# Performance work log

Measured on AMD Instinct MI355X. Metric: run time of the kernel, lower is better.

The kernel has to match this reference:

```python
import jax, jax.numpy as jnp
import numpy as np

NH, NKV, HD = 32, 8, 64  # num heads, num kv heads, head_dim


def apply_rope(x, fc):
    # x: [B,S,H,D], fc: [S, D//2, 2]
    b, s, h, d = x.shape
    xr = x.reshape(b, s, h, d // 2, 2)
    fc = fc.reshape(1, s, 1, d // 2, 2)
    out = jnp.stack([
        xr[..., 0] * fc[..., 0] - xr[..., 1] * fc[..., 1],
        xr[..., 1] * fc[..., 0] + xr[..., 0] * fc[..., 1],
    ], axis=-1)
    return out.reshape(b, s, h, d)


def setup_inputs() -> dict:
    key = jax.random.key(0)
    k0, k1, k2 = jax.random.split(key, 3)
    B, S, H = 1, 2048, 2048
    x = jax.random.normal(k0, (B, S, H), jnp.float32)
    # rotary cos/sin table: [S, HD//2, 2]
    pos = jnp.arange(S, dtype=jnp.float32)
    inv_freq = 1.0 / (10000.0 ** (jnp.arange(0, HD, 2, dtype=jnp.float32) / HD))
    ang = pos[:, None] * inv_freq[None, :]
    freqs_cis = jnp.stack([jnp.cos(ang), jnp.sin(ang)], axis=-1)
    # causal bool mask [1,1,S,S]
    mask = jnp.tril(jnp.ones((S, S), dtype=bool))[None, None]
    scale = H ** -0.5
    Wqkv = jax.random.normal(k1, ((NH + 2 * NKV) * HD, H), jnp.float32) * scale
    Wo = jax.random.normal(k2, (H, H), jnp.float32) * scale
    return {"x": x, "freqs_cis": freqs_cis, "mask": mask, "Wqkv": Wqkv, "Wo": Wo}


def reference(x, freqs_cis, mask, Wqkv, Wo):
    B, S, H = x.shape
    g = NH // NKV  # GQA group size
    qkv = x @ Wqkv.T  # [B,S,(NH+2*NKV)*HD]
    q, k, v = jnp.split(qkv, [NH * HD, NH * HD + NKV * HD], axis=-1)
    q = q.reshape(B, S, NH, HD)
    k = k.reshape(B, S, NKV, HD)
    v = v.reshape(B, S, NKV, HD)
    q = apply_rope(q, freqs_cis)
    k = apply_rope(k, freqs_cis)
    # group query heads by shared kv head instead of repeat_interleave on K/V
    q = q.reshape(B, S, NKV, g, HD)
    scores = jnp.einsum('bskgd,btkd->bkgst', q, k) * (HD ** -0.5)
    scores = jnp.where(mask.reshape(1, 1, 1, S, S), scores, -jnp.inf)
    p = jax.nn.softmax(scores, axis=-1)
    y = jnp.einsum('bkgst,btkd->bskgd', p, v).reshape(B, S, H)
    return y @ Wo.T
```

## Files before the change

### kernel.cpp

```cpp
#include <hip/hip_runtime.h>
#include <stdint.h>

typedef unsigned short ushort_t;
typedef __attribute__((ext_vector_type(8))) short s8v;
typedef __attribute__((ext_vector_type(4))) float f4v;

#define NH 32
#define NKV 8
#define HD 64
#define S_LEN 2048
#define HID 2048
#define DQKV 3072

#define QSCALE 0.18033688011112042f

__device__ __forceinline__ ushort_t f2b(float f) {
  union { float f; unsigned u; } v; v.f = f;
  unsigned r = v.u + 0x7FFFu + ((v.u >> 16) & 1u);
  return (ushort_t)(r >> 16);
}
__device__ __forceinline__ float b2f(ushort_t h) {
  union { unsigned u; float f; } v; v.u = ((unsigned)h) << 16;
  return v.f;
}
__device__ __forceinline__ unsigned cvtpk(float lo, float hi) {
  unsigned r;
  asm("v_cvt_pk_bf16_f32 %0, %1, %2" : "=v"(r) : "v"(lo), "v"(hi));
  return r;
}

__global__ void cvt3(const float* __restrict__ a, const float* __restrict__ b,
                     const float* __restrict__ c, ushort_t* __restrict__ oa,
                     ushort_t* __restrict__ ob, ushort_t* __restrict__ oc) {
  const int n1 = 1048576, n2 = 1572864;
  int i = blockIdx.x * blockDim.x + threadIdx.x;
  const float* in; ushort_t* out; int j;
  if (i < n1) { in = a; out = oa; j = i; }
  else if (i < n1 + n2) { in = b; out = ob; j = i - n1; }
  else { in = c; out = oc; j = i - n1 - n2; }
  float4 v = ((const float4*)in)[j];
  uint2 p;
  p.x = cvtpk(v.x, v.y);
  p.y = cvtpk(v.z, v.w);
  ((uint2*)out)[j] = p;
}

__global__ __launch_bounds__(256) void gemm_bt_sk(
    const ushort_t* __restrict__ A, const ushort_t* __restrict__ B,
    ushort_t* __restrict__ C0, ushort_t* __restrict__ C1, int M, int N, int K) {
  __shared__ ushort_t sA[128 * 32];
  __shared__ ushort_t sB[128 * 32];
  const int tid = threadIdx.x;
  const int wave = tid >> 6, lane = tid & 63;
  const int bm = blockIdx.y * 128, bn = blockIdx.x * 128;
  const int wm = (wave >> 1) * 64, wn = (wave & 1) * 64;
  const int srow = wave * 16 + (lane >> 2);
  const int scol = (lane & 3) * 8;
  const int fr = lane & 15, fg = lane >> 4;
  const int khalf = K >> 1;
  const int kbeg = blockIdx.z * khalf;
  ushort_t* C = blockIdx.z ? C1 : C0;

  f4v acc[4][4];
#pragma unroll
  for (int m = 0; m < 4; ++m)
#pragma unroll
    for (int n = 0; n < 4; ++n) acc[m][n] = (f4v){0.f, 0.f, 0.f, 0.f};

  for (int k0 = kbeg; k0 < kbeg + khalf; k0 += 32) {
    __syncthreads();
#pragma unroll
    for (int it = 0; it < 2; ++it) {
      int r = it * 64 + srow;
      __builtin_amdgcn_global_load_lds(
          (const __attribute__((address_space(1))) void*)(A + (size_t)(bm + r) * K + k0 + scol),
          (__attribute__((address_space(3))) void*)(&sA[(it * 64 + wave * 16) * 32]),
          16, 0, 0);
      __builtin_amdgcn_global_load_lds(
          (const __attribute__((address_space(1))) void*)(B + (size_t)(bn + r) * K + k0 + scol),
          (__attribute__((address_space(3))) void*)(&sB[(it * 64 + wave * 16) * 32]),
          16, 0, 0);
    }
    __syncthreads();

    s8v af[4], bf[4];
#pragma unroll
    for (int m = 0; m < 4; ++m)
      af[m] = *(const s8v*)&sA[(wm + m * 16 + fr) * 32 + fg * 8];
#pragma unroll
    for (int n = 0; n < 4; ++n)
      bf[n] = *(const s8v*)&sB[(wn + n * 16 + fr) * 32 + fg * 8];
#pragma unroll
    for (int m = 0; m < 4; ++m)
#pragma unroll
      for (int n = 0; n < 4; ++n)
        acc[m][n] = __builtin_amdgcn_mfma_f32_16x16x32_bf16(af[m], bf[n], acc[m][n], 0, 0, 0);
  }

#pragma unroll
  for (int m = 0; m < 4; ++m)
#pragma unroll
    for (int n = 0; n < 4; ++n)
#pragma unroll
      for (int rr = 0; rr < 4; ++rr) {
        int row = bm + wm + m * 16 + fg * 4 + rr;
        int col = bn + wn + n * 16 + fr;
        C[(size_t)row * N + col] = f2b(acc[m][n][rr]);
      }
}

__global__ void add2(const ushort_t* __restrict__ a, const ushort_t* __restrict__ b,
                     float* __restrict__ out) {
  int i = blockIdx.x * blockDim.x + threadIdx.x;
  uint2 pa = ((const uint2*)a)[i];
  uint2 pb = ((const uint2*)b)[i];
  float4 o;
  o.x = b2f((ushort_t)(pa.x & 0xFFFF)) + b2f((ushort_t)(pb.x & 0xFFFF));
  o.y = b2f((ushort_t)(pa.x >> 16))    + b2f((ushort_t)(pb.x >> 16));
  o.z = b2f((ushort_t)(pa.y & 0xFFFF)) + b2f((ushort_t)(pb.y & 0xFFFF));
  o.w = b2f((ushort_t)(pa.y >> 16))    + b2f((ushort_t)(pb.y >> 16));
  ((float4*)out)[i] = o;
}

__global__ void rope_qk(const ushort_t* __restrict__ P0, const ushort_t* __restrict__ P1,
                        const float* __restrict__ fc,
                        ushort_t* __restrict__ Qb, ushort_t* __restrict__ Kb) {
  int tid = blockIdx.x * blockDim.x + threadIdx.x;
  if (tid >= S_LEN * 160) return;
  int s = tid / 160, c = tid - s * 160;
  int h = c >> 2, part = c & 3;
  size_t off = (size_t)s * DQKV + h * 64 + part * 16;
  s8v a0 = *(const s8v*)(P0 + off);
  s8v a1 = *(const s8v*)(P0 + off + 8);
  s8v b0 = *(const s8v*)(P1 + off);
  s8v b1 = *(const s8v*)(P1 + off + 8);
  float xv[16];
#pragma unroll
  for (int i = 0; i < 8; ++i) {
    xv[i]     = b2f((ushort_t)a0[i]) + b2f((ushort_t)b0[i]);
    xv[8 + i] = b2f((ushort_t)a1[i]) + b2f((ushort_t)b1[i]);
  }
  const float* fp = fc + s * 64 + part * 16;
  float fv[16];
  ((float4*)fv)[0] = ((const float4*)fp)[0];
  ((float4*)fv)[1] = ((const float4*)fp)[1];
  ((float4*)fv)[2] = ((const float4*)fp)[2];
  ((float4*)fv)[3] = ((const float4*)fp)[3];
  const float scale = (h < NH) ? QSCALE : 1.0f;
  ushort_t obuf[16];
#pragma unroll
  for (int i = 0; i < 8; ++i) {
    float x0 = xv[2 * i], x1 = xv[2 * i + 1];
    float cs = fv[2 * i], sn = fv[2 * i + 1];
    obuf[2 * i]     = f2b((x0 * cs - x1 * sn) * scale);
    obuf[2 * i + 1] = f2b((x1 * cs + x0 * sn) * scale);
  }
  ushort_t* dst;
  if (h < NH) dst = Qb + ((size_t)s * NH + h) * 64 + part * 16;
  else        dst = Kb + ((size_t)s * NKV + (h - NH)) * 64 + part * 16;
  *(s8v*)dst = *(const s8v*)&obuf[0];
  *(s8v*)(dst + 8) = *(const s8v*)&obuf[8];
}

__global__ void transp_v(const ushort_t* __restrict__ P0, const ushort_t* __restrict__ P1,
                         ushort_t* __restrict__ Vt) {
  __shared__ float t[32][33];
  int hd0 = blockIdx.x * 32, s0 = blockIdx.y * 32;
#pragma unroll
  for (int k = 0; k < 4; ++k) {
    int sy = threadIdx.y + k * 8;
    size_t off = (size_t)(s0 + sy) * DQKV + 2560 + hd0 + threadIdx.x;
    t[sy][threadIdx.x] = b2f(P0[off]) + b2f(P1[off]);
  }
  __syncthreads();
#pragma unroll
  for (int k = 0; k < 4; ++k) {
    int hy = threadIdx.y + k * 8;
    Vt[(size_t)(hd0 + hy) * S_LEN + s0 + threadIdx.x] = f2b(t[threadIdx.x][hy]);
  }
}

__device__ __forceinline__ void softmax_pack(f4v (&sc)[4], float& m, float& l,
                                             f4v (&y)[4], s8v (&pf)[2], int fg) {
  float pmax = sc[0][0];
#pragma unroll
  for (int n = 0; n < 4; ++n)
#pragma unroll
    for (int r = 0; r < 4; ++r) pmax = fmaxf(pmax, sc[n][r]);
  pmax = fmaxf(pmax, __shfl_xor(pmax, 16));
  pmax = fmaxf(pmax, __shfl_xor(pmax, 32));
  if (!__all(pmax <= m + 8.f)) {
    float mn = fmaxf(m, pmax);
    float al = exp2f(m - mn);
    m = mn;
    l *= al;
    float aly[4];
#pragma unroll
    for (int rr = 0; rr < 4; ++rr) aly[rr] = __shfl(al, fg * 4 + rr);
#pragma unroll
    for (int d = 0; d < 4; ++d)
#pragma unroll
      for (int rr = 0; rr < 4; ++rr) y[d][rr] *= aly[rr];
  }
  float rs = 0.f;
#pragma unroll
  for (int n = 0; n < 4; ++n)
#pragma unroll
    for (int r = 0; r < 4; ++r) {
      float p = exp2f(sc[n][r] - m);
      sc[n][r] = p;
      rs += p;
    }
  l += rs;
#pragma unroll
  for (int c = 0; c < 2; ++c) {
    unsigned wb[4];
    wb[0] = cvtpk(sc[2 * c][0], sc[2 * c][1]);
    wb[1] = cvtpk(sc[2 * c][2], sc[2 * c][3]);
    wb[2] = cvtpk(sc[2 * c + 1][0], sc[2 * c + 1][1]);
    wb[3] = cvtpk(sc[2 * c + 1][2], sc[2 * c + 1][3]);
    pf[c] = *(const s8v*)&wb[0];
  }
}

__device__ __forceinline__ void finalize_y(f4v (&y)[4], float l, int q0, int head,
                                           int fr, int fg, ushort_t* __restrict__ Y) {
  l += __shfl_xor(l, 16);
  l += __shfl_xor(l, 32);
  float linv[4];
#pragma unroll
  for (int rr = 0; rr < 4; ++rr) linv[rr] = 1.f / __shfl(l, fg * 4 + rr);
#pragma unroll
  for (int d = 0; d < 4; ++d)
#pragma unroll
    for (int rr = 0; rr < 4; ++rr)
      Y[(size_t)(q0 + fg * 4 + rr) * HID + head * 64 + d * 16 + fr] =
          f2b(y[d][rr] * linv[rr]);
}

__global__ __launch_bounds__(128) void attn(
    const ushort_t* __restrict__ Q, const ushort_t* __restrict__ Kc,
    const ushort_t* __restrict__ Vt, ushort_t* __restrict__ Y) {
  __shared__ float Lm[2][64];
  __shared__ float Ll[2][64];
  __shared__ float Ly[2][64][17];
  const int head = blockIdx.y, kvh = head >> 2;
  const int w = threadIdx.x >> 6;
  const int lane = threadIdx.x & 63;
  const int fr = lane & 15, fg = lane >> 4;
  const int jA = 127 - (int)blockIdx.x;
  const int jB = (int)blockIdx.x;
  const int q0A = jA * 16, q0B = jB * 16;
  const int ntA = (q0A >> 6) + 1, ntB = (q0B >> 6) + 1;

  s8v qfA[2], qfB[2];
#pragma unroll
  for (int c = 0; c < 2; ++c) {
    qfA[c] = *(const s8v*)(Q + ((size_t)(q0A + fr) * NH + head) * 64 + c * 32 + fg * 8);
    qfB[c] = *(const s8v*)(Q + ((size_t)(q0B + fr) * NH + head) * 64 + c * 32 + fg * 8);
  }

  float mA = -3.0e38f, lA = 0.f, mB = -3.0e38f, lB = 0.f;
  f4v yA[4], yB[4];
#pragma unroll
  for (int d = 0; d < 4; ++d) {
    yA[d] = (f4v){0.f, 0.f, 0.f, 0.f};
    yB[d] = (f4v){0.f, 0.f, 0.f, 0.f};
  }

  for (int t = w; t < ntA; t += 2) {
    const int kv0 = t * 64;
    const bool doB = (t < ntB);
    s8v kf[4][2];
#pragma unroll
    for (int n = 0; n < 4; ++n) {
      const int krow = kv0 + 32 * (n >> 1) + 8 * (fr >> 2) + 4 * (n & 1) + (fr & 3);
      const ushort_t* kb = Kc + ((size_t)krow * NKV + kvh) * 64 + fg * 8;
      kf[n][0] = *(const s8v*)kb;
      kf[n][1] = *(const s8v*)(kb + 32);
    }
    f4v scA[4], scB[4];
#pragma unroll
    for (int n = 0; n < 4; ++n) {
      f4v a = (f4v){0.f, 0.f, 0.f, 0.f};
      a = __builtin_amdgcn_mfma_f32_16x16x32_bf16(kf[n][0], qfA[0], a, 0, 0, 0);
      a = __builtin_amdgcn_mfma_f32_16x16x32_bf16(kf[n][1], qfA[1], a, 0, 0, 0);
      scA[n] = a;
    }
    if (doB) {
#pragma unroll
      for (int n = 0; n < 4; ++n) {
        f4v a = (f4v){0.f, 0.f, 0.f, 0.f};
        a = __builtin_amdgcn_mfma_f32_16x16x32_bf16(kf[n][0], qfB[0], a, 0, 0, 0);
        a = __builtin_amdgcn_mfma_f32_16x16x32_bf16(kf[n][1], qfB[1], a, 0, 0, 0);
        scB[n] = a;
      }
    }
    if (t == ntA - 1) {
#pragma unroll
      for (int n = 0; n < 4; ++n)
#pragma unroll
        for (int r = 0; r < 4; ++r) {
          int kv = kv0 + 32 * (n >> 1) + 8 * fg + 4 * (n & 1) + r;
          if (kv > q0A + fr) scA[n][r] = -1e30f;
        }
    }
    if (doB && t == ntB - 1) {
#pragma unroll
      for (int n = 0; n < 4; ++n)
#pragma unroll
        for (int r = 0; r < 4; ++r) {
          int kv = kv0 + 32 * (n >> 1) + 8 * fg + 4 * (n & 1) + r;
          if (kv > q0B + fr) scB[n][r] = -1e30f;
        }
    }
    s8v pfA[2], pfB[2];
    softmax_pack(scA, mA, lA, yA, pfA, fg);
    if (doB) softmax_pack(scB, mB, lB, yB, pfB, fg);
#pragma unroll
    for (int d = 0; d < 4; ++d) {
      const ushort_t* vb = Vt + ((size_t)(kvh * 64 + d * 16 + fr)) * S_LEN + kv0 + fg * 8;
      s8v vf0 = *(const s8v*)vb;
      s8v vf1 = *(const s8v*)(vb + 32);
      yA[d] = __builtin_amdgcn_mfma_f32_16x16x32_bf16(pfA[0], vf0, yA[d], 0, 0, 0);
      yA[d] = __builtin_amdgcn_mfma_f32_16x16x32_bf16(pfA[1], vf1, yA[d], 0, 0, 0);
      if (doB) {
        yB[d] = __builtin_amdgcn_mfma_f32_16x16x32_bf16(pfB[0], vf0, yB[d], 0, 0, 0);
        yB[d] = __builtin_amdgcn_mfma_f32_16x16x32_bf16(pfB[1], vf1, yB[d], 0, 0, 0);
      }
    }
  }

  if (w == 0) {
    Lm[1][lane] = mB; Ll[1][lane] = lB;
#pragma unroll
    for (int d = 0; d < 4; ++d)
#pragma unroll
      for (int rr = 0; rr < 4; ++rr) Ly[1][lane][d * 4 + rr] = yB[d][rr];
  } else {
    Lm[0][lane] = mA; Ll[0][lane] = lA;
#pragma unroll
    for (int d = 0; d < 4; ++d)
#pragma unroll
      for (int rr = 0; rr < 4; ++rr) Ly[0][lane][d * 4 + rr] = yA[d][rr];
  }
  __syncthreads();
  if (w == 0) {
    float m1 = Lm[0][lane], l1 = Ll[0][lane];
    float mm = fmaxf(mA, m1);
    float s0 = exp2f(mA - mm), s1 = exp2f(m1 - mm);
    float lm = lA * s0 + l1 * s1;
    float s0y[4], s1y[4];
#pragma unroll
    for (int rr = 0; rr < 4; ++rr) {
      s0y[rr] = __shfl(s0, fg * 4 + rr);
      s1y[rr] = __shfl(s1, fg * 4 + rr);
    }
#pragma unroll
    for (int d = 0; d < 4; ++d)
#pragma unroll
      for (int rr = 0; rr < 4; ++rr)
        yA[d][rr] = yA[d][rr] * s0y[rr] + Ly[0][lane][d * 4 + rr] * s1y[rr];
    finalize_y(yA, lm, q0A, head, fr, fg, Y);
  } else {
    float m1 = Lm[1][lane], l1 = Ll[1][lane];
    float mm = fmaxf(mB, m1);
    float s0 = exp2f(mB - mm), s1 = exp2f(m1 - mm);
    float lm = lB * s0 + l1 * s1;
    float s0y[4], s1y[4];
#pragma unroll
    for (int rr = 0; rr < 4; ++rr) {
      s0y[rr] = __shfl(s0, fg * 4 + rr);
      s1y[rr] = __shfl(s1, fg * 4 + rr);
    }
#pragma unroll
    for (int d = 0; d < 4; ++d)
#pragma unroll
      for (int rr = 0; rr < 4; ++rr)
        yB[d][rr] = yB[d][rr] * s0y[rr] + Ly[1][lane][d * 4 + rr] * s1y[rr];
    finalize_y(yB, lm, q0B, head, fr, fg, Y);
  }
}

extern "C" void kernel_launch(void* const* d_in, const int* in_sizes, int n_in,
                              void* d_out, int out_size, void* d_ws, size_t ws_size,
                              hipStream_t stream) {
  const float* x    = (const float*)d_in[0];
  const float* fc   = (const float*)d_in[1];
  const float* wqkv = (const float*)d_in[3];
  const float* wo   = (const float*)d_in[4];
  float* out = (float*)d_out;

  char* ws = (char*)d_ws;
  ushort_t* xb    = (ushort_t*)(ws);
  ushort_t* wqkvb = (ushort_t*)(ws + 8388608);
  ushort_t* Qb    = (ushort_t*)(ws + 8388608);
  ushort_t* Kb    = (ushort_t*)(ws + 16777216);
  ushort_t* Vtb   = (ushort_t*)(ws + 18874368);
  ushort_t* wob   = (ushort_t*)(ws + 20971520);
  ushort_t* P0    = (ushort_t*)(ws + 29360128);
  ushort_t* P1    = (ushort_t*)(ws + 41943040);
  ushort_t* G0    = (ushort_t*)(ws + 29360128);
  ushort_t* G1    = (ushort_t*)(ws + 37748736);
  ushort_t* Yb    = xb;

  cvt3<<<14336, 256, 0, stream>>>(x, wqkv, wo, xb, wqkvb, wob);

  gemm_bt_sk<<<dim3(24, 16, 2), 256, 0, stream>>>(xb, wqkvb, P0, P1, 2048, 3072, 2048);

  rope_qk<<<1280, 256, 0, stream>>>(P0, P1, fc, Qb, Kb);
  transp_v<<<dim3(16, 64), dim3(32, 8), 0, stream>>>(P0, P1, Vtb);

  attn<<<dim3(64, 32), 128, 0, stream>>>(Qb, Kb, Vtb, Yb);

  gemm_bt_sk<<<dim3(16, 16, 2), 256, 0, stream>>>(Yb, wob, G0, G1, 2048, 2048, 2048);

  add2<<<4096, 256, 0, stream>>>(G0, G1, out);
}
```

Measured before the change: 309.9 us.

## Pre-pack K and V into MFMA fragment order for coalesced attention loads

The rope kernel now writes K, and the V transpose kernel now writes V, directly in a packed per-head, per-64-row-tile layout that matches the MFMA operand fragments. In that layout each lane's 16-byte load in the attention loop is contiguous across the wavefront. Before, K loads were strided across rows and V loads were strided by sequence length. The cost is more complex index math in the producer kernels, and pack_v now writes with only half its threads.

New measurement: 273.6 us. 1.13x faster.

```diff
diff --git a/kernel.cpp b/kernel.cpp
--- a/kernel.cpp
+++ b/kernel.cpp
@@ -11,6 +11,10 @@
 #define S_LEN 2048
 #define HID 2048
 #define DQKV 3072
+
+#define PK_CHUNK 512
+#define PK_TILE 4096
+#define PK_HEAD 131072
 
 #define QSCALE 0.18033688011112042f
 
@@ -124,7 +128,7 @@
 
 __global__ void rope_qk(const ushort_t* __restrict__ P0, const ushort_t* __restrict__ P1,
                         const float* __restrict__ fc,
-                        ushort_t* __restrict__ Qb, ushort_t* __restrict__ Kb) {
+                        ushort_t* __restrict__ Qb, ushort_t* __restrict__ Kp) {
   int tid = blockIdx.x * blockDim.x + threadIdx.x;
   if (tid >= S_LEN * 160) return;
   int s = tid / 160, c = tid - s * 160;
@@ -155,15 +159,26 @@
     obuf[2 * i]     = f2b((x0 * cs - x1 * sn) * scale);
     obuf[2 * i + 1] = f2b((x1 * cs + x0 * sn) * scale);
   }
-  ushort_t* dst;
-  if (h < NH) dst = Qb + ((size_t)s * NH + h) * 64 + part * 16;
-  else        dst = Kb + ((size_t)s * NKV + (h - NH)) * 64 + part * 16;
-  *(s8v*)dst = *(const s8v*)&obuf[0];
-  *(s8v*)(dst + 8) = *(const s8v*)&obuf[8];
-}
-
-__global__ void transp_v(const ushort_t* __restrict__ P0, const ushort_t* __restrict__ P1,
-                         ushort_t* __restrict__ Vt) {
+  if (h < NH) {
+    ushort_t* dst = Qb + ((size_t)s * NH + h) * 64 + part * 16;
+    *(s8v*)dst = *(const s8v*)&obuf[0];
+    *(s8v*)(dst + 8) = *(const s8v*)&obuf[8];
+  } else {
+    const int kvh = h - NH;
+    const int t_ = s >> 6, rloc = s & 63;
+    const int n_ = 2 * (rloc >> 5) + ((rloc >> 2) & 1);
+    const int fr_ = 4 * ((rloc >> 3) & 3) + (rloc & 3);
+    const int c_ = part >> 1;
+    const int fg0 = (part & 1) * 2;
+    ushort_t* dst = Kp + (size_t)kvh * PK_HEAD + t_ * PK_TILE +
+                    (n_ * 2 + c_) * PK_CHUNK + (fg0 * 16 + fr_) * 8;
+    *(s8v*)dst = *(const s8v*)&obuf[0];
+    *(s8v*)(dst + 128) = *(const s8v*)&obuf[8];
+  }
+}
+
+__global__ void pack_v(const ushort_t* __restrict__ P0, const ushort_t* __restrict__ P1,
+                       ushort_t* __restrict__ Vp) {
   __shared__ float t[32][33];
   int hd0 = blockIdx.x * 32, s0 = blockIdx.y * 32;
 #pragma unroll
@@ -173,10 +188,18 @@
     t[sy][threadIdx.x] = b2f(P0[off]) + b2f(P1[off]);
   }
   __syncthreads();
-#pragma unroll
-  for (int k = 0; k < 4; ++k) {
-    int hy = threadIdx.y + k * 8;
-    Vt[(size_t)(hd0 + hy) * S_LEN + s0 + threadIdx.x] = f2b(t[threadIdx.x][hy]);
+  if (threadIdx.y < 4) {
+    const int fg = threadIdx.y;
+    const int hdl = (hd0 & 32) + threadIdx.x;
+    const int kvh = hd0 >> 6;
+    const int d = hdl >> 4, fr = hdl & 15;
+    const int tt = s0 >> 6, cc = (s0 >> 5) & 1;
+    ushort_t ob[8];
+#pragma unroll
+    for (int j = 0; j < 8; ++j) ob[j] = f2b(t[fg * 8 + j][threadIdx.x]);
+    ushort_t* dst = Vp + (size_t)kvh * PK_HEAD + tt * PK_TILE +
+                    (d * 2 + cc) * PK_CHUNK + (fg * 16 + fr) * 8;
+    *(s8v*)dst = *(const s8v*)&ob[0];
   }
 }
 
@@ -239,8 +262,8 @@
 }
 
 __global__ __launch_bounds__(128) void attn(
-    const ushort_t* __restrict__ Q, const ushort_t* __restrict__ Kc,
-    const ushort_t* __restrict__ Vt, ushort_t* __restrict__ Y) {
+    const ushort_t* __restrict__ Q, const ushort_t* __restrict__ Kp,
+    const ushort_t* __restrict__ Vp, ushort_t* __restrict__ Y) {
   __shared__ float Lm[2][64];
   __shared__ float Ll[2][64];
   __shared__ float Ly[2][64][17];
@@ -252,6 +275,8 @@
   const int jB = (int)blockIdx.x;
   const int q0A = jA * 16, q0B = jB * 16;
   const int ntA = (q0A >> 6) + 1, ntB = (q0B >> 6) + 1;
+  const ushort_t* Kh = Kp + (size_t)kvh * PK_HEAD + lane * 8;
+  const ushort_t* Vh = Vp + (size_t)kvh * PK_HEAD + lane * 8;
 
   s8v qfA[2], qfB[2];
 #pragma unroll
@@ -271,13 +296,13 @@
   for (int t = w; t < ntA; t += 2) {
     const int kv0 = t * 64;
     const bool doB = (t < ntB);
+    const ushort_t* kt = Kh + t * PK_TILE;
+    const ushort_t* vt = Vh + t * PK_TILE;
     s8v kf[4][2];
 #pragma unroll
     for (int n = 0; n < 4; ++n) {
-      const int krow = kv0 + 32 * (n >> 1) + 8 * (fr >> 2) + 4 * (n & 1) + (fr & 3);
-      const ushort_t* kb = Kc + ((size_t)krow * NKV + kvh) * 64 + fg * 8;
-      kf[n][0] = *(const s8v*)kb;
-      kf[n][1] = *(const s8v*)(kb + 32);
+      kf[n][0] = *(const s8v*)(kt + (n * 2 + 0) * PK_CHUNK);
+      kf[n][1] = *(const s8v*)(kt + (n * 2 + 1) * PK_CHUNK);
     }
     f4v scA[4], scB[4];
 #pragma unroll
@@ -319,9 +344,8 @@
     if (doB) softmax_pack(scB, mB, lB, yB, pfB, fg);
 #pragma unroll
     for (int d = 0; d < 4; ++d) {
-      const ushort_t* vb = Vt + ((size_t)(kvh * 64 + d * 16 + fr)) * S_LEN + kv0 + fg * 8;
-      s8v vf0 = *(const s8v*)vb;
-      s8v vf1 = *(const s8v*)(vb + 32);
+      s8v vf0 = *(const s8v*)(vt + (d * 2 + 0) * PK_CHUNK);
+      s8v vf1 = *(const s8v*)(vt + (d * 2 + 1) * PK_CHUNK);
       yA[d] = __builtin_amdgcn_mfma_f32_16x16x32_bf16(pfA[0], vf0, yA[d], 0, 0, 0);
       yA[d] = __builtin_amdgcn_mfma_f32_16x16x32_bf16(pfA[1], vf1, yA[d], 0, 0, 0);
       if (doB) {
@@ -395,8 +419,8 @@
   ushort_t* xb    = (ushort_t*)(ws);
   ushort_t* wqkvb = (ushort_t*)(ws + 8388608);
   ushort_t* Qb    = (ushort_t*)(ws + 8388608);
-  ushort_t* Kb    = (ushort_t*)(ws + 16777216);
-  ushort_t* Vtb   = (ushort_t*)(ws + 18874368);
+  ushort_t* Kpb   = (ushort_t*)(ws + 16777216);
+  ushort_t* Vpb   = (ushort_t*)(ws + 18874368);
   ushort_t* wob   = (ushort_t*)(ws + 20971520);
   ushort_t* P0    = (ushort_t*)(ws + 29360128);
   ushort_t* P1    = (ushort_t*)(ws + 41943040);
@@ -408,10 +432,10 @@
 
   gemm_bt_sk<<<dim3(24, 16, 2), 256, 0, stream>>>(xb, wqkvb, P0, P1, 2048, 3072, 2048);
 
-  rope_qk<<<1280, 256, 0, stream>>>(P0, P1, fc, Qb, Kb);
-  transp_v<<<dim3(16, 64), dim3(32, 8), 0, stream>>>(P0, P1, Vtb);
-
-  attn<<<dim3(64, 32), 128, 0, stream>>>(Qb, Kb, Vtb, Yb);
+  rope_qk<<<1280, 256, 0, stream>>>(P0, P1, fc, Qb, Kpb);
+  pack_v<<<dim3(16, 64), dim3(32, 8), 0, stream>>>(P0, P1, Vpb);
+
+  attn<<<dim3(64, 32), 128, 0, stream>>>(Qb, Kpb, Vpb, Yb);
 
   gemm_bt_sk<<<dim3(16, 16, 2), 256, 0, stream>>>(Yb, wob, G0, G1, 2048, 2048, 2048);
 
```
